# Optimization experiments

Measured on AMD Instinct MI355X. Metric: run time of the kernel, lower is better.

The kernel has to match this reference:

```python
import jax, jax.numpy as jnp
import numpy as np

B, S, D, P, R, NL = 16, 2048, 1024, 8192, 16, 64  # docs, seq, d_model, pairs, n_relations, n_label_pairs
MAX_SPAN = 32


def setup_inputs() -> dict:
    key = jax.random.key(0)
    ks = jax.random.split(key, 8)
    tokvecs = jax.random.normal(ks[0], (B, S, D), dtype=jnp.float32)
    batch_idx = jax.random.randint(ks[1], (P,), 0, B, dtype=jnp.int32)
    e1s = jax.random.randint(ks[2], (P,), 0, S - MAX_SPAN, dtype=jnp.int32)
    e1e = e1s + 1 + jax.random.randint(ks[3], (P,), 0, MAX_SPAN - 1, dtype=jnp.int32)
    e2s = jax.random.randint(ks[4], (P,), 0, S - MAX_SPAN, dtype=jnp.int32)
    e2e = e2s + 1 + jax.random.randint(ks[5], (P,), 0, MAX_SPAN - 1, dtype=jnp.int32)
    rel_idx = jax.random.randint(ks[6], (P,), 0, NL, dtype=jnp.int32)
    # multi-hot relationship-inclusion table (0/1 entries, as built in __init__)
    rel_table = (jax.random.uniform(ks[7], (NL, R)) < 0.25).astype(jnp.float32)
    return {
        "tokvecs": tokvecs,
        "batch_idx": batch_idx,
        "ent1_start": e1s,
        "ent1_end": e1e,
        "ent2_start": e2s,
        "ent2_end": e2e,
        "rel_idx": rel_idx,
        "rel_table": rel_table,
    }


def _span_mean(cs, b, s, e):
    # cs: [B, S+1, D] exclusive prefix sums; span mean = (cs[e] - cs[s]) / (e - s)
    seg = cs[b, e] - cs[b, s]                      # [P, D]
    return seg / (e - s)[:, None].astype(seg.dtype)


def reference(tokvecs, batch_idx, ent1_start, ent1_end, ent2_start, ent2_end, rel_idx, rel_table):
    Bn, Sn, Dn = tokvecs.shape
    # exclusive prefix sum along sequence -> O(1) mean per span instead of ragged gathers
    cs = jnp.concatenate(
        [jnp.zeros((Bn, 1, Dn), tokvecs.dtype), jnp.cumsum(tokvecs, axis=1)], axis=1
    )                                               # [B, S+1, D]
    m1 = _span_mean(cs, batch_idx, ent1_start, ent1_end)   # [P, D]
    m2 = _span_mean(cs, batch_idx, ent2_start, ent2_end)   # [P, D]
    rel = rel_table[rel_idx]                                # [P, R]
    return jnp.concatenate([m1, m2, rel], axis=-1)          # [P, 2D + R]
```

## Files before the change

kernel.cpp:

```cpp
#include <hip/hip_runtime.h>

#define S_LEN      2048
#define D_DIM      1024
#define R_DIM      16
#define OUT_STRIDE 2064
#define NKEYS      32768
#define GROUP      8


__global__ __launch_bounds__(256) void zero_hist(int* __restrict__ h) {
    h[blockIdx.x * 256 + threadIdx.x] = 0;
}

__global__ __launch_bounds__(256) void hist_jobs(
    const int* __restrict__ bidx, const int* __restrict__ e1s,
    const int* __restrict__ e2s, int* __restrict__ hist, int njobs)
{
    const int j = blockIdx.x * 256 + threadIdx.x;
    if (j >= njobs) return;
    const int p = j >> 1;
    const int s = (j & 1) ? e2s[p] : e1s[p];
    atomicAdd(hist + bidx[p] * S_LEN + s, 1);
}

__global__ __launch_bounds__(1024) void scan_hist(int* __restrict__ hist) {
    __shared__ int lds[1024];
    const int t = threadIdx.x;
    int v[32];
    int sum = 0;
#pragma unroll
    for (int i = 0; i < 32; ++i) { v[i] = hist[t * 32 + i]; sum += v[i]; }
    lds[t] = sum;
    __syncthreads();
    for (int off = 1; off < 1024; off <<= 1) {
        int x = (t >= off) ? lds[t - off] : 0;
        __syncthreads();
        lds[t] += x;
        __syncthreads();
    }
    int run = (t == 0) ? 0 : lds[t - 1];
#pragma unroll
    for (int i = 0; i < 32; ++i) { int c = v[i]; hist[t * 32 + i] = run; run += c; }
}

__global__ __launch_bounds__(256) void scatter_jobs(
    const int* __restrict__ bidx, const int* __restrict__ e1s,
    const int* __restrict__ e2s, int* __restrict__ cursor,
    int* __restrict__ sorted, int njobs)
{
    const int j = blockIdx.x * 256 + threadIdx.x;
    if (j >= njobs) return;
    const int p = j >> 1;
    const int s = (j & 1) ? e2s[p] : e1s[p];
    const int pos = atomicAdd(cursor + bidx[p] * S_LEN + s, 1);
    sorted[pos] = j;
}

__global__ __launch_bounds__(256) void gather_grouped(
    const float* __restrict__ tok,
    const int*   __restrict__ sorted,
    const int*   __restrict__ bidx,
    const int*   __restrict__ e1s, const int* __restrict__ e1e,
    const int*   __restrict__ e2s, const int* __restrict__ e2e,
    const int*   __restrict__ ridx,
    const float* __restrict__ rtab,
    float*       __restrict__ out)
{
    const int g = blockIdx.x;
    const int t = threadIdx.x;

    int jp[GROUP], jh[GROUP], js[GROUP], je[GROUP];
    int mins = 0x7fffffff, maxe = 0;
#pragma unroll
    for (int i = 0; i < GROUP; ++i) {
        const int id = __builtin_amdgcn_readfirstlane(sorted[g * GROUP + i]);
        const int p  = id >> 1;
        const int h  = id & 1;
        const int b  = __builtin_amdgcn_readfirstlane(bidx[p]);
        const int s  = __builtin_amdgcn_readfirstlane(h ? e2s[p] : e1s[p]);
        const int e  = __builtin_amdgcn_readfirstlane(h ? e2e[p] : e1e[p]);
        jp[i] = p; jh[i] = h;
        js[i] = b * S_LEN + s;
        je[i] = b * S_LEN + e;
        mins  = min(mins, js[i]);
        maxe  = max(maxe, je[i]);
    }

    float4 acc[GROUP];
#pragma unroll
    for (int i = 0; i < GROUP; ++i) acc[i] = make_float4(0.f, 0.f, 0.f, 0.f);

    const float4* src = reinterpret_cast<const float4*>(tok) +
                        (size_t)mins * (D_DIM / 4) + t;
    for (int r = mins; r < maxe; ++r) {
        const float4 v = *src;
        src += D_DIM / 4;
#pragma unroll
        for (int i = 0; i < GROUP; ++i) {
            if (r >= js[i] && r < je[i]) {
                acc[i].x += v.x; acc[i].y += v.y;
                acc[i].z += v.z; acc[i].w += v.w;
            }
        }
    }

#pragma unroll
    for (int i = 0; i < GROUP; ++i) {
        const float inv = 1.0f / (float)(je[i] - js[i]);
        const float4 o = make_float4(acc[i].x * inv, acc[i].y * inv,
                                     acc[i].z * inv, acc[i].w * inv);
        float* dst = out + (size_t)jp[i] * OUT_STRIDE + jh[i] * D_DIM + t * 4;
        *reinterpret_cast<float4*>(dst) = o;
        if (jh[i] == 0 && t < 4) {
            const float4 rv = *reinterpret_cast<const float4*>(
                rtab + ridx[jp[i]] * R_DIM + t * 4);
            *reinterpret_cast<float4*>(
                out + (size_t)jp[i] * OUT_STRIDE + 2 * D_DIM + t * 4) = rv;
        }
    }
}

extern "C" void kernel_launch(void* const* d_in, const int* in_sizes, int n_in,
                              void* d_out, int out_size, void* d_ws, size_t ws_size,
                              hipStream_t stream) {
    const float* tok  = (const float*)d_in[0];
    const int*   bidx = (const int*)d_in[1];
    const int*   e1s  = (const int*)d_in[2];
    const int*   e1e  = (const int*)d_in[3];
    const int*   e2s  = (const int*)d_in[4];
    const int*   e2e  = (const int*)d_in[5];
    const int*   ridx = (const int*)d_in[6];
    const float* rtab = (const float*)d_in[7];
    float*       out  = (float*)d_out;

    const int P     = in_sizes[1];
    const int njobs = 2 * P;

    int* cursor = (int*)d_ws;
    int* sorted = (int*)d_ws + NKEYS;

    zero_hist<<<NKEYS / 256, 256, 0, stream>>>(cursor);
    hist_jobs<<<(njobs + 255) / 256, 256, 0, stream>>>(bidx, e1s, e2s, cursor, njobs);
    scan_hist<<<1, 1024, 0, stream>>>(cursor);
    scatter_jobs<<<(njobs + 255) / 256, 256, 0, stream>>>(bidx, e1s, e2s, cursor,
                                                          sorted, njobs);
    gather_grouped<<<njobs / GROUP, 256, 0, stream>>>(
        tok, sorted, bidx, e1s, e1e, e2s, e2e, ridx, rtab, out);
}
```

Baseline: 305.6 us.

## Split gather across D halves, prefetch rows, and use weighted FMA accumulation

Each group of eight span jobs is now handled by two 128-thread blocks, each covering one half of the feature dimension, which doubles the number of blocks. The row loop is unrolled by four with a software-prefetched next batch of rows, so loads overlap with compute. The per-row branch is replaced by multiplying each row by a precomputed 1/len weight (zero outside the span), which also removes the final division. Block indices are permuted to spread neighbouring groups across XCDs. The trade-off is extra FMAs on rows where the weight is zero, plus more registers and clamped redundant loads at the tail.

```diff
diff --git a/kernel.cpp b/kernel.cpp
--- a/kernel.cpp
+++ b/kernel.cpp
@@ -56,7 +56,7 @@
     sorted[pos] = j;
 }
 
-__global__ __launch_bounds__(256) void gather_grouped(
+__global__ __launch_bounds__(128) void gather_grouped3(
     const float* __restrict__ tok,
     const int*   __restrict__ sorted,
     const int*   __restrict__ bidx,
@@ -66,10 +66,14 @@
     const float* __restrict__ rtab,
     float*       __restrict__ out)
 {
-    const int g = blockIdx.x;
-    const int t = threadIdx.x;
+    const int blk = blockIdx.x;
+    const int w  = (blk & 7) * (gridDim.x >> 3) + (blk >> 3);
+    const int g  = w >> 1;
+    const int ch = w & 1;
+    const int t  = threadIdx.x;
 
-    int jp[GROUP], jh[GROUP], js[GROUP], je[GROUP];
+    int   jp[GROUP], jh[GROUP], js[GROUP], je[GROUP];
+    float jw[GROUP];
     int mins = 0x7fffffff, maxe = 0;
 #pragma unroll
     for (int i = 0; i < GROUP; ++i) {
@@ -82,6 +86,7 @@
         jp[i] = p; jh[i] = h;
         js[i] = b * S_LEN + s;
         je[i] = b * S_LEN + e;
+        jw[i] = 1.0f / (float)(e - s);
         mins  = min(mins, js[i]);
         maxe  = max(maxe, je[i]);
     }
@@ -90,28 +95,46 @@
 #pragma unroll
     for (int i = 0; i < GROUP; ++i) acc[i] = make_float4(0.f, 0.f, 0.f, 0.f);
 
-    const float4* src = reinterpret_cast<const float4*>(tok) +
-                        (size_t)mins * (D_DIM / 4) + t;
-    for (int r = mins; r < maxe; ++r) {
-        const float4 v = *src;
-        src += D_DIM / 4;
+    const float4* base = reinterpret_cast<const float4*>(tok) +
+                         (size_t)mins * (D_DIM / 4) + ch * 128 + t;
+    const int nrows = maxe - mins;
+    const int rmax  = nrows - 1;
+    const int niter = (nrows + 3) >> 2;
+
+    float4 cur[4];
+#pragma unroll
+    for (int k = 0; k < 4; ++k)
+        cur[k] = base[(size_t)min(k, rmax) * (D_DIM / 4)];
+
+    for (int it = 0; it < niter; ++it) {
+        const int r0 = it * 4;
+        float4 nxt[4];
+#pragma unroll
+        for (int k = 0; k < 4; ++k)
+            nxt[k] = base[(size_t)min(r0 + 4 + k, rmax) * (D_DIM / 4)];
+
+        const int gr = mins + r0;
 #pragma unroll
         for (int i = 0; i < GROUP; ++i) {
-            if (r >= js[i] && r < je[i]) {
-                acc[i].x += v.x; acc[i].y += v.y;
-                acc[i].z += v.z; acc[i].w += v.w;
-            }
+            const float w0 = (gr + 0 >= js[i] && gr + 0 < je[i]) ? jw[i] : 0.f;
+            const float w1 = (gr + 1 >= js[i] && gr + 1 < je[i]) ? jw[i] : 0.f;
+            const float w2 = (gr + 2 >= js[i] && gr + 2 < je[i]) ? jw[i] : 0.f;
+            const float w3 = (gr + 3 >= js[i] && gr + 3 < je[i]) ? jw[i] : 0.f;
+            acc[i].x += cur[0].x * w0 + cur[1].x * w1 + cur[2].x * w2 + cur[3].x * w3;
+            acc[i].y += cur[0].y * w0 + cur[1].y * w1 + cur[2].y * w2 + cur[3].y * w3;
+            acc[i].z += cur[0].z * w0 + cur[1].z * w1 + cur[2].z * w2 + cur[3].z * w3;
+            acc[i].w += cur[0].w * w0 + cur[1].w * w1 + cur[2].w * w2 + cur[3].w * w3;
         }
+#pragma unroll
+        for (int k = 0; k < 4; ++k) cur[k] = nxt[k];
     }
 
 #pragma unroll
     for (int i = 0; i < GROUP; ++i) {
-        const float inv = 1.0f / (float)(je[i] - js[i]);
-        const float4 o = make_float4(acc[i].x * inv, acc[i].y * inv,
-                                     acc[i].z * inv, acc[i].w * inv);
-        float* dst = out + (size_t)jp[i] * OUT_STRIDE + jh[i] * D_DIM + t * 4;
-        *reinterpret_cast<float4*>(dst) = o;
-        if (jh[i] == 0 && t < 4) {
+        float* dst = out + (size_t)jp[i] * OUT_STRIDE + jh[i] * D_DIM +
+                     ch * 512 + t * 4;
+        *reinterpret_cast<float4*>(dst) = acc[i];
+        if (ch == 0 && jh[i] == 0 && t < 4) {
             const float4 rv = *reinterpret_cast<const float4*>(
                 rtab + ridx[jp[i]] * R_DIM + t * 4);
             *reinterpret_cast<float4*>(
@@ -144,6 +167,7 @@
     scan_hist<<<1, 1024, 0, stream>>>(cursor);
     scatter_jobs<<<(njobs + 255) / 256, 256, 0, stream>>>(bidx, e1s, e2s, cursor,
                                                           sorted, njobs);
-    gather_grouped<<<njobs / GROUP, 256, 0, stream>>>(
+    const int nblocks = (njobs / GROUP) * 2;
+    gather_grouped3<<<nblocks, 128, 0, stream>>>(
         tok, sorted, bidx, e1s, e1e, e2s, e2e, ridx, rtab, out);
 }
```

Result: faster. 265.4 us (-13.1%).
